# Kernel tuning notes

Measured on AMD Instinct MI355X. Metric: run time of the kernel, lower is better.

## Reference

```python
import jax, jax.numpy as jnp
import numpy as np

N = 10000          # num nodes
E = 640000         # num edges (avg degree 64)
IN_CH = 128
OUT_CH = 128


def setup_inputs() -> dict:
    key = jax.random.key(0)
    k_x, k_ei, k_ea, k_w1, k_b1, k_w2, k_b2 = jax.random.split(key, 7)
    x = jax.random.normal(k_x, (N, IN_CH), dtype=jnp.float32)
    edge_index = jax.random.randint(k_ei, (2, E), 0, N, dtype=jnp.int64)
    edge_attr = jax.random.uniform(k_ea, (E,), dtype=jnp.float32)
    # MLP params: Linear(2*in, out) -> ReLU -> Linear(out, out), stored as [in, out]
    s1 = 1.0 / np.sqrt(2 * IN_CH)
    s2 = 1.0 / np.sqrt(OUT_CH)
    W1 = jax.random.uniform(k_w1, (2 * IN_CH, OUT_CH), jnp.float32, -s1, s1)
    b1 = jax.random.uniform(k_b1, (OUT_CH,), jnp.float32, -s1, s1)
    W2 = jax.random.uniform(k_w2, (OUT_CH, OUT_CH), jnp.float32, -s2, s2)
    b2 = jax.random.uniform(k_b2, (OUT_CH,), jnp.float32, -s2, s2)
    return {"x": x, "edge_index": edge_index, "edge_attr": edge_attr,
            "W1": W1, "b1": b1, "W2": W2, "b2": b2}


def reference(x, edge_index, edge_attr, W1, b1, W2, b2):
    row, col = edge_index[0], edge_index[1]
    # message: scale sender feature by edge_attr, concat with receiver feature, 2-layer MLP
    x_i = x[row] * edge_attr[:, None]          # [E, in]
    x_j = x[col]                               # [E, in]
    combined = jnp.concatenate([x_i, x_j], axis=1)  # [E, 2*in]
    h = jax.nn.relu(combined @ W1 + b1)        # [E, out]
    messages = h @ W2 + b2                     # [E, out]
    # sum aggregation: scatter-add messages into receiving nodes (col)
    out = jnp.zeros((x.shape[0], messages.shape[1]), dtype=messages.dtype)
    out = out.at[col].add(messages)
    return out
```

## Files before the change

### kernel.cpp

```cpp
#include <hip/hip_runtime.h>

#define C 128
#define NPB 16
#define CAP 128
#define OVF_MAX 65536
#define EPT1 16
#define GSH 5
#define G (1 << GSH)
#define CAPB 3072
#define MAXBIN 512

__device__ __forceinline__ unsigned bf16_bits(float x) {
    unsigned u = __float_as_uint(x);
    u += 0x7FFFu + ((u >> 16) & 1u);
    return u >> 16;
}
__device__ __forceinline__ float bf16f(unsigned short b) {
    return __uint_as_float(((unsigned)b) << 16);
}

__global__ void fused_pre_kernel(const float* __restrict__ x, const float* __restrict__ W1,
                                 unsigned short* __restrict__ P16, float* __restrict__ Q,
                                 const int* __restrict__ ei, const float* __restrict__ attr,
                                 uint2* __restrict__ bins, int* __restrict__ bin_cursor,
                                 int* __restrict__ ovf_cnt, int2* __restrict__ ovf,
                                 int N, int E, int PBLK, int NBIN) {
    if ((int)blockIdx.x < PBLK) {
        __shared__ int hist[MAXBIN];
        __shared__ int boff[MAXBIN];
        for (int i = threadIdx.x; i < NBIN; i += 256) { hist[i] = 0; boff[i] = 0; }
        __syncthreads();
        const int base = ((int)blockIdx.x * 256 + (int)threadIdx.x) * EPT1;
        const int rem = (base < E) ? min(EPT1, E - base) : 0;
        const bool vec = (rem == EPT1) && ((E & 3) == 0);
        if (vec) {
#pragma unroll
            for (int j0 = 0; j0 < EPT1; j0 += 4) {
                const int4 c = *(const int4*)(ei + (size_t)E + base + j0);
                atomicAdd(&hist[c.x >> GSH], 1);
                atomicAdd(&hist[c.y >> GSH], 1);
                atomicAdd(&hist[c.z >> GSH], 1);
                atomicAdd(&hist[c.w >> GSH], 1);
            }
        } else {
            for (int j = 0; j < rem; ++j)
                atomicAdd(&hist[ei[(size_t)E + base + j] >> GSH], 1);
        }
        __syncthreads();
        for (int i = threadIdx.x; i < NBIN; i += 256) {
            const int c = hist[i];
            int b = 0;
            if (c) {
                const int cp = (c + 7) & ~7;
                b = atomicAdd(&bin_cursor[i], cp);
                for (int k = c; k < cp; ++k)
                    if (b + k < CAPB)
                        bins[(size_t)i * CAPB + b + k] = make_uint2(0u, 0xFFFFFFFFu);
            }
            hist[i] = b;
        }
        __syncthreads();
        if (vec) {
#pragma unroll
            for (int j0 = 0; j0 < EPT1; j0 += 4) {
                const int4 r = *(const int4*)(ei + base + j0);
                const int4 c = *(const int4*)(ei + (size_t)E + base + j0);
                const float4 a = *(const float4*)(attr + base + j0);
                const int rr[4] = {r.x, r.y, r.z, r.w};
                const int cc[4] = {c.x, c.y, c.z, c.w};
                const float aa[4] = {a.x, a.y, a.z, a.w};
#pragma unroll
                for (int j = 0; j < 4; ++j) {
                    const int bin = cc[j] >> GSH;
                    const int idx = hist[bin] + atomicAdd(&boff[bin], 1);
                    const unsigned pk = (bf16_bits(aa[j]) << 16) | (unsigned)rr[j];
                    if (idx < CAPB) {
                        bins[(size_t)bin * CAPB + idx] = make_uint2(pk, (unsigned)cc[j]);
                    } else {
                        const int o = atomicAdd(ovf_cnt, 1);
                        if (o < OVF_MAX) ovf[o] = make_int2(cc[j], (int)pk);
                    }
                }
            }
        } else {
            for (int j = 0; j < rem; ++j) {
                const int row = ei[base + j], colv = ei[(size_t)E + base + j];
                const int bin = colv >> GSH;
                const int idx = hist[bin] + atomicAdd(&boff[bin], 1);
                const unsigned pk = (bf16_bits(attr[base + j]) << 16) | (unsigned)row;
                if (idx < CAPB) {
                    bins[(size_t)bin * CAPB + idx] = make_uint2(pk, (unsigned)colv);
                } else {
                    const int o = atomicAdd(ovf_cnt, 1);
                    if (o < OVF_MAX) ovf[o] = make_int2(colv, (int)pk);
                }
            }
        }
    } else {
        __shared__ float xs[NPB][C];
        const int pb = (int)blockIdx.x - PBLK;
        const int n0 = pb * NPB;
        const int tt = threadIdx.x & (C - 1);
        const int half = threadIdx.x >> 7;
        for (int i = threadIdx.x; i < NPB * C; i += 256) {
            const int gi = n0 * C + i;
            xs[0][i] = (gi < N * C) ? x[gi] : 0.f;
        }
        __syncthreads();
        const float* __restrict__ Wb = W1 + (half ? (C * C) : 0) + tt;
        float acc[NPB] = {};
        for (int k = 0; k < C; ++k) {
            const float w = Wb[k * C];
#pragma unroll
            for (int j = 0; j < NPB; ++j)
                acc[j] = fmaf(xs[j][k], w, acc[j]);
        }
#pragma unroll
        for (int j = 0; j < NPB; ++j)
            if (n0 + j < N) {
                if (half) Q[(size_t)(n0 + j) * C + tt] = acc[j];
                else      P16[(size_t)(n0 + j) * C + tt] = (unsigned short)bf16_bits(acc[j]);
            }
    }
}

__global__ void bin_scatter_kernel(const uint2* __restrict__ bins, const int* __restrict__ bin_cursor,
                                   unsigned* __restrict__ sorted, int* __restrict__ cursor,
                                   int* __restrict__ ovf_cnt, int2* __restrict__ ovf, int N) {
    __shared__ int off[G];
    const int b = blockIdx.x;
    const int n0 = b << GSH;
    if (threadIdx.x < G) off[threadIdx.x] = 0;
    __syncthreads();
    const int cnt = min(bin_cursor[b], CAPB);
    const uint2* __restrict__ src = bins + (size_t)b * CAPB;
    for (int i = threadIdx.x; i < cnt; i += 256) {
        const uint2 e = src[i];
        const unsigned noff = e.y - (unsigned)n0;
        if (noff < (unsigned)G) {
            const int pos = atomicAdd(&off[noff], 1);
            if (pos < CAP) {
                sorted[(size_t)e.y * CAP + pos] = e.x;
            } else {
                const int o = atomicAdd(ovf_cnt, 1);
                if (o < OVF_MAX) ovf[o] = make_int2((int)e.y, (int)e.x);
            }
        }
    }
    __syncthreads();
    if (threadIdx.x < G && n0 + (int)threadIdx.x < N)
        cursor[n0 + threadIdx.x] = min(off[threadIdx.x], CAP);
}

__global__ void agg_out_kernel(const unsigned* __restrict__ sorted, const int* __restrict__ cursor,
                               const unsigned short* __restrict__ P16, const float* __restrict__ Q,
                               const float* __restrict__ b1, const float* __restrict__ W2,
                               const float* __restrict__ b2,
                               const int* __restrict__ ovf_cnt, const int2* __restrict__ ovf,
                               float* __restrict__ out, int N) {
    __shared__ float4 part[2][4][32];
    __shared__ float hs[2][C];
    const int t = threadIdx.x;
    const int j = t >> 7;
    const int slice = (t >> 5) & 3;
    const int ch4 = t & 31;
    const int n = blockIdx.x * 2 + j;

    float4 acc = make_float4(0.f, 0.f, 0.f, 0.f);
    float4 qb = acc;
    int deg = 0;
    int mcnt = 0;
    if (n < N) {
        deg = cursor[n];
        const float4 q4  = *(const float4*)(Q + (size_t)n * C + (ch4 << 2));
        const float4 b14 = *(const float4*)(b1 + (ch4 << 2));
        qb = make_float4(q4.x + b14.x, q4.y + b14.y, q4.z + b14.z, q4.w + b14.w);
        const int cnt = min(deg, CAP);
        const unsigned* __restrict__ buf = sorted + (size_t)n * CAP;
        const int chunk = (cnt + 3) >> 2;
        const int s0 = min(slice * chunk, cnt);
        const int s1 = min(s0 + chunk, cnt);
        int i = s0;
        for (; i + 4 <= s1; i += 4) {
            const unsigned v0 = buf[i], v1 = buf[i + 1], v2 = buf[i + 2], v3 = buf[i + 3];
            const ushort4 p0 = *(const ushort4*)(P16 + (((size_t)(v0 & 0xFFFFu)) << 7) + (ch4 << 2));
            const ushort4 p1 = *(const ushort4*)(P16 + (((size_t)(v1 & 0xFFFFu)) << 7) + (ch4 << 2));
            const ushort4 p2 = *(const ushort4*)(P16 + (((size_t)(v2 & 0xFFFFu)) << 7) + (ch4 << 2));
            const ushort4 p3 = *(const ushort4*)(P16 + (((size_t)(v3 & 0xFFFFu)) << 7) + (ch4 << 2));
            const float a0 = __uint_as_float(v0 & 0xFFFF0000u);
            const float a1 = __uint_as_float(v1 & 0xFFFF0000u);
            const float a2 = __uint_as_float(v2 & 0xFFFF0000u);
            const float a3 = __uint_as_float(v3 & 0xFFFF0000u);
            acc.x += fmaxf(fmaf(a0, bf16f(p0.x), qb.x), 0.f) + fmaxf(fmaf(a1, bf16f(p1.x), qb.x), 0.f)
                   + fmaxf(fmaf(a2, bf16f(p2.x), qb.x), 0.f) + fmaxf(fmaf(a3, bf16f(p3.x), qb.x), 0.f);
            acc.y += fmaxf(fmaf(a0, bf16f(p0.y), qb.y), 0.f) + fmaxf(fmaf(a1, bf16f(p1.y), qb.y), 0.f)
                   + fmaxf(fmaf(a2, bf16f(p2.y), qb.y), 0.f) + fmaxf(fmaf(a3, bf16f(p3.y), qb.y), 0.f);
            acc.z += fmaxf(fmaf(a0, bf16f(p0.z), qb.z), 0.f) + fmaxf(fmaf(a1, bf16f(p1.z), qb.z), 0.f)
                   + fmaxf(fmaf(a2, bf16f(p2.z), qb.z), 0.f) + fmaxf(fmaf(a3, bf16f(p3.z), qb.z), 0.f);
            acc.w += fmaxf(fmaf(a0, bf16f(p0.w), qb.w), 0.f) + fmaxf(fmaf(a1, bf16f(p1.w), qb.w), 0.f)
                   + fmaxf(fmaf(a2, bf16f(p2.w), qb.w), 0.f) + fmaxf(fmaf(a3, bf16f(p3.w), qb.w), 0.f);
        }
        for (; i < s1; ++i) {
            const unsigned v = buf[i];
            const ushort4 p = *(const ushort4*)(P16 + (((size_t)(v & 0xFFFFu)) << 7) + (ch4 << 2));
            const float a = __uint_as_float(v & 0xFFFF0000u);
            acc.x += fmaxf(fmaf(a, bf16f(p.x), qb.x), 0.f);
            acc.y += fmaxf(fmaf(a, bf16f(p.y), qb.y), 0.f);
            acc.z += fmaxf(fmaf(a, bf16f(p.z), qb.z), 0.f);
            acc.w += fmaxf(fmaf(a, bf16f(p.w), qb.w), 0.f);
        }
        if (slice == 0) {
            const int oc = min(*ovf_cnt, OVF_MAX);
            for (int o = 0; o < oc; ++o) {
                const int2 v = ovf[o];
                if (v.x == n) {
                    ++mcnt;
                    const unsigned u = (unsigned)v.y;
                    const ushort4 p = *(const ushort4*)(P16 + (((size_t)(u & 0xFFFFu)) << 7) + (ch4 << 2));
                    const float a = __uint_as_float(u & 0xFFFF0000u);
                    acc.x += fmaxf(fmaf(a, bf16f(p.x), qb.x), 0.f);
                    acc.y += fmaxf(fmaf(a, bf16f(p.y), qb.y), 0.f);
                    acc.z += fmaxf(fmaf(a, bf16f(p.z), qb.z), 0.f);
                    acc.w += fmaxf(fmaf(a, bf16f(p.w), qb.w), 0.f);
                }
            }
        }
    }
    part[j][slice][ch4] = acc;
    __syncthreads();
    if (slice == 0 && n < N) {
        const float4 r0 = part[j][0][ch4], r1 = part[j][1][ch4];
        const float4 r2 = part[j][2][ch4], r3 = part[j][3][ch4];
        float4 h;
        h.x = r0.x + r1.x + r2.x + r3.x;
        h.y = r0.y + r1.y + r2.y + r3.y;
        h.z = r0.z + r1.z + r2.z + r3.z;
        h.w = r0.w + r1.w + r2.w + r3.w;
        *(float4*)(&hs[j][ch4 << 2]) = h;
    }
    __syncthreads();
    float4 o = make_float4(0.f, 0.f, 0.f, 0.f);
    if (n < N) {
        const int k0 = slice << 5;
#pragma unroll 8
        for (int k = k0; k < k0 + 32; ++k) {
            const float hv = hs[j][k];
            const float4 w = *(const float4*)(W2 + (size_t)k * C + (ch4 << 2));
            o.x = fmaf(hv, w.x, o.x);
            o.y = fmaf(hv, w.y, o.y);
            o.z = fmaf(hv, w.z, o.z);
            o.w = fmaf(hv, w.w, o.w);
        }
    }
    __syncthreads();
    part[j][slice][ch4] = o;
    __syncthreads();
    if (slice == 0 && n < N) {
        const float4 r0 = part[j][0][ch4], r1 = part[j][1][ch4];
        const float4 r2 = part[j][2][ch4], r3 = part[j][3][ch4];
        const float4 b24 = *(const float4*)(b2 + (ch4 << 2));
        const float d = (float)(deg + mcnt);
        float4 res;
        res.x = fmaf(d, b24.x, r0.x + r1.x + r2.x + r3.x);
        res.y = fmaf(d, b24.y, r0.y + r1.y + r2.y + r3.y);
        res.z = fmaf(d, b24.z, r0.z + r1.z + r2.z + r3.z);
        res.w = fmaf(d, b24.w, r0.w + r1.w + r2.w + r3.w);
        *(float4*)(out + (size_t)n * C + (ch4 << 2)) = res;
    }
}

extern "C" void kernel_launch(void* const* d_in, const int* in_sizes, int n_in,
                              void* d_out, int out_size, void* d_ws, size_t ws_size,
                              hipStream_t stream) {
    const float* x    = (const float*)d_in[0];
    const int*   ei   = (const int*)d_in[1];
    const float* attr = (const float*)d_in[2];
    const float* W1   = (const float*)d_in[3];
    const float* b1   = (const float*)d_in[4];
    const float* W2   = (const float*)d_in[5];
    const float* b2   = (const float*)d_in[6];
    float* out = (float*)d_out;

    const int N = in_sizes[0] / C;
    const int E = in_sizes[2];
    const int NBIN = (N + G - 1) >> GSH;

    char* ws = (char*)d_ws;
    unsigned short* P16 = (unsigned short*)ws;  ws += (size_t)N * C * sizeof(unsigned short);
    ws = (char*)(((uintptr_t)ws + 15) & ~(uintptr_t)15);
    float*    Q       = (float*)ws;     ws += (size_t)N * C * sizeof(float);
    unsigned* sorted  = (unsigned*)ws;  ws += (size_t)N * CAP * sizeof(unsigned);
    uint2*    bins    = (uint2*)ws;     ws += (size_t)NBIN * CAPB * sizeof(uint2);
    int2*     ovf     = (int2*)ws;      ws += (size_t)OVF_MAX * sizeof(int2);
    int*      cursor  = (int*)ws;       ws += (size_t)N * sizeof(int);
    int*      bin_cursor = (int*)ws;    ws += (size_t)NBIN * sizeof(int);
    int*      ovf_cnt = (int*)ws;

    hipMemsetAsync(bin_cursor, 0, ((size_t)NBIN + 1) * sizeof(int), stream);

    const int PBLK = (E + 256 * EPT1 - 1) / (256 * EPT1);
    const int PB = (N + NPB - 1) / NPB;
    fused_pre_kernel<<<PBLK + PB, 256, 0, stream>>>(x, W1, P16, Q, ei, attr,
                                                    bins, bin_cursor, ovf_cnt, ovf,
                                                    N, E, PBLK, NBIN);
    bin_scatter_kernel<<<NBIN, 256, 0, stream>>>(bins, bin_cursor, sorted, cursor,
                                                 ovf_cnt, ovf, N);
    agg_out_kernel<<<(N + 1) / 2, 256, 0, stream>>>(sorted, cursor, P16, Q, b1, W2, b2,
                                                    ovf_cnt, ovf, out, N);
}
```

Baseline: 143.0 us.

## Split aggregation and W2 GEMM into separate kernels with wider gathers

Moves the per-node W2 projection out of the aggregation kernel into a separate tiled GEMM kernel that handles 16 nodes per block and reuses each W2 load across 8 rows. The aggregation kernel now stages the node's edge list in shared memory and gathers 8 bf16 channels per thread with 16-byte loads, using 8 edge groups instead of 4. This removes the per-node re-read of all of W2 and the extra barriers in the old fused tail. In exchange it adds an intermediate H buffer round trip through global memory and one more kernel launch.

Measured after the change: 137.3 us. -4.0%, faster.

```diff
diff --git a/kernel.cpp b/kernel.cpp
--- a/kernel.cpp
+++ b/kernel.cpp
@@ -14,9 +14,6 @@
     unsigned u = __float_as_uint(x);
     u += 0x7FFFu + ((u >> 16) & 1u);
     return u >> 16;
-}
-__device__ __forceinline__ float bf16f(unsigned short b) {
-    return __uint_as_float(((unsigned)b) << 16);
 }
 
 __global__ void fused_pre_kernel(const float* __restrict__ x, const float* __restrict__ W1,
@@ -152,120 +149,140 @@
         cursor[n0 + threadIdx.x] = min(off[threadIdx.x], CAP);
 }
 
-__global__ void agg_out_kernel(const unsigned* __restrict__ sorted, const int* __restrict__ cursor,
-                               const unsigned short* __restrict__ P16, const float* __restrict__ Q,
-                               const float* __restrict__ b1, const float* __restrict__ W2,
-                               const float* __restrict__ b2,
-                               const int* __restrict__ ovf_cnt, const int2* __restrict__ ovf,
-                               float* __restrict__ out, int N) {
-    __shared__ float4 part[2][4][32];
-    __shared__ float hs[2][C];
+__global__ void agg_kernel(const unsigned* __restrict__ sorted, const int* __restrict__ cursor,
+                           const unsigned short* __restrict__ P16, const float* __restrict__ Q,
+                           const float* __restrict__ b1,
+                           const int* __restrict__ ovf_cnt, const int2* __restrict__ ovf,
+                           float* __restrict__ H, int* __restrict__ degw, int N) {
+    __shared__ unsigned ebuf[2][CAP];
+    __shared__ float4 red[2][8][32];
     const int t = threadIdx.x;
     const int j = t >> 7;
-    const int slice = (t >> 5) & 3;
-    const int ch4 = t & 31;
+    const int tl = t & 127;
+    const int grp = tl >> 4;
+    const int ch8 = t & 15;
     const int n = blockIdx.x * 2 + j;
 
-    float4 acc = make_float4(0.f, 0.f, 0.f, 0.f);
-    float4 qb = acc;
-    int deg = 0;
-    int mcnt = 0;
+    int deg = 0, cnt = 0, mcnt = 0;
     if (n < N) {
         deg = cursor[n];
-        const float4 q4  = *(const float4*)(Q + (size_t)n * C + (ch4 << 2));
-        const float4 b14 = *(const float4*)(b1 + (ch4 << 2));
-        qb = make_float4(q4.x + b14.x, q4.y + b14.y, q4.z + b14.z, q4.w + b14.w);
-        const int cnt = min(deg, CAP);
-        const unsigned* __restrict__ buf = sorted + (size_t)n * CAP;
-        const int chunk = (cnt + 3) >> 2;
-        const int s0 = min(slice * chunk, cnt);
+        cnt = min(deg, CAP);
+        for (int i = tl; i < cnt; i += 128)
+            ebuf[j][i] = sorted[(size_t)n * CAP + i];
+    }
+    __syncthreads();
+
+    float4 acc0 = make_float4(0.f, 0.f, 0.f, 0.f);
+    float4 acc1 = acc0;
+    if (n < N) {
+        const float4 qlo = *(const float4*)(Q + (size_t)n * C + (ch8 << 3));
+        const float4 qhi = *(const float4*)(Q + (size_t)n * C + (ch8 << 3) + 4);
+        const float4 blo = *(const float4*)(b1 + (ch8 << 3));
+        const float4 bhi = *(const float4*)(b1 + (ch8 << 3) + 4);
+        const float4 qb0 = make_float4(qlo.x + blo.x, qlo.y + blo.y, qlo.z + blo.z, qlo.w + blo.w);
+        const float4 qb1 = make_float4(qhi.x + bhi.x, qhi.y + bhi.y, qhi.z + bhi.z, qhi.w + bhi.w);
+        const int chunk = (cnt + 7) >> 3;
+        const int s0 = min(grp * chunk, cnt);
         const int s1 = min(s0 + chunk, cnt);
         int i = s0;
-        for (; i + 4 <= s1; i += 4) {
-            const unsigned v0 = buf[i], v1 = buf[i + 1], v2 = buf[i + 2], v3 = buf[i + 3];
-            const ushort4 p0 = *(const ushort4*)(P16 + (((size_t)(v0 & 0xFFFFu)) << 7) + (ch4 << 2));
-            const ushort4 p1 = *(const ushort4*)(P16 + (((size_t)(v1 & 0xFFFFu)) << 7) + (ch4 << 2));
-            const ushort4 p2 = *(const ushort4*)(P16 + (((size_t)(v2 & 0xFFFFu)) << 7) + (ch4 << 2));
-            const ushort4 p3 = *(const ushort4*)(P16 + (((size_t)(v3 & 0xFFFFu)) << 7) + (ch4 << 2));
-            const float a0 = __uint_as_float(v0 & 0xFFFF0000u);
-            const float a1 = __uint_as_float(v1 & 0xFFFF0000u);
-            const float a2 = __uint_as_float(v2 & 0xFFFF0000u);
-            const float a3 = __uint_as_float(v3 & 0xFFFF0000u);
-            acc.x += fmaxf(fmaf(a0, bf16f(p0.x), qb.x), 0.f) + fmaxf(fmaf(a1, bf16f(p1.x), qb.x), 0.f)
-                   + fmaxf(fmaf(a2, bf16f(p2.x), qb.x), 0.f) + fmaxf(fmaf(a3, bf16f(p3.x), qb.x), 0.f);
-            acc.y += fmaxf(fmaf(a0, bf16f(p0.y), qb.y), 0.f) + fmaxf(fmaf(a1, bf16f(p1.y), qb.y), 0.f)
-                   + fmaxf(fmaf(a2, bf16f(p2.y), qb.y), 0.f) + fmaxf(fmaf(a3, bf16f(p3.y), qb.y), 0.f);
-            acc.z += fmaxf(fmaf(a0, bf16f(p0.z), qb.z), 0.f) + fmaxf(fmaf(a1, bf16f(p1.z), qb.z), 0.f)
-                   + fmaxf(fmaf(a2, bf16f(p2.z), qb.z), 0.f) + fmaxf(fmaf(a3, bf16f(p3.z), qb.z), 0.f);
-            acc.w += fmaxf(fmaf(a0, bf16f(p0.w), qb.w), 0.f) + fmaxf(fmaf(a1, bf16f(p1.w), qb.w), 0.f)
-                   + fmaxf(fmaf(a2, bf16f(p2.w), qb.w), 0.f) + fmaxf(fmaf(a3, bf16f(p3.w), qb.w), 0.f);
+        for (; i + 2 <= s1; i += 2) {
+            const unsigned e0 = ebuf[j][i], e1 = ebuf[j][i + 1];
+            const uint4 p0 = *(const uint4*)(P16 + (((size_t)(e0 & 0xFFFFu)) << 7) + (ch8 << 3));
+            const uint4 p1 = *(const uint4*)(P16 + (((size_t)(e1 & 0xFFFFu)) << 7) + (ch8 << 3));
+            const float a0 = __uint_as_float(e0 & 0xFFFF0000u);
+            const float a1 = __uint_as_float(e1 & 0xFFFF0000u);
+            acc0.x += fmaxf(fmaf(a0, __uint_as_float(p0.x << 16),         qb0.x), 0.f)
+                    + fmaxf(fmaf(a1, __uint_as_float(p1.x << 16),         qb0.x), 0.f);
+            acc0.y += fmaxf(fmaf(a0, __uint_as_float(p0.x & 0xFFFF0000u), qb0.y), 0.f)
+                    + fmaxf(fmaf(a1, __uint_as_float(p1.x & 0xFFFF0000u), qb0.y), 0.f);
+            acc0.z += fmaxf(fmaf(a0, __uint_as_float(p0.y << 16),         qb0.z), 0.f)
+                    + fmaxf(fmaf(a1, __uint_as_float(p1.y << 16),         qb0.z), 0.f);
+            acc0.w += fmaxf(fmaf(a0, __uint_as_float(p0.y & 0xFFFF0000u), qb0.w), 0.f)
+                    + fmaxf(fmaf(a1, __uint_as_float(p1.y & 0xFFFF0000u), qb0.w), 0.f);
+            acc1.x += fmaxf(fmaf(a0, __uint_as_float(p0.z << 16),         qb1.x), 0.f)
+                    + fmaxf(fmaf(a1, __uint_as_float(p1.z << 16),         qb1.x), 0.f);
+            acc1.y += fmaxf(fmaf(a0, __uint_as_float(p0.z & 0xFFFF0000u), qb1.y), 0.f)
+                    + fmaxf(fmaf(a1, __uint_as_float(p1.z & 0xFFFF0000u), qb1.y), 0.f);
+            acc1.z += fmaxf(fmaf(a0, __uint_as_float(p0.w << 16),         qb1.z), 0.f)
+                    + fmaxf(fmaf(a1, __uint_as_float(p1.w << 16),         qb1.z), 0.f);
+            acc1.w += fmaxf(fmaf(a0, __uint_as_float(p0.w & 0xFFFF0000u), qb1.w), 0.f)
+                    + fmaxf(fmaf(a1, __uint_as_float(p1.w & 0xFFFF0000u), qb1.w), 0.f);
         }
         for (; i < s1; ++i) {
-            const unsigned v = buf[i];
-            const ushort4 p = *(const ushort4*)(P16 + (((size_t)(v & 0xFFFFu)) << 7) + (ch4 << 2));
-            const float a = __uint_as_float(v & 0xFFFF0000u);
-            acc.x += fmaxf(fmaf(a, bf16f(p.x), qb.x), 0.f);
-            acc.y += fmaxf(fmaf(a, bf16f(p.y), qb.y), 0.f);
-            acc.z += fmaxf(fmaf(a, bf16f(p.z), qb.z), 0.f);
-            acc.w += fmaxf(fmaf(a, bf16f(p.w), qb.w), 0.f);
-        }
-        if (slice == 0) {
+            const unsigned e0 = ebuf[j][i];
+            const uint4 p0 = *(const uint4*)(P16 + (((size_t)(e0 & 0xFFFFu)) << 7) + (ch8 << 3));
+            const float a0 = __uint_as_float(e0 & 0xFFFF0000u);
+            acc0.x += fmaxf(fmaf(a0, __uint_as_float(p0.x << 16),         qb0.x), 0.f);
+            acc0.y += fmaxf(fmaf(a0, __uint_as_float(p0.x & 0xFFFF0000u), qb0.y), 0.f);
+            acc0.z += fmaxf(fmaf(a0, __uint_as_float(p0.y << 16),         qb0.z), 0.f);
+            acc0.w += fmaxf(fmaf(a0, __uint_as_float(p0.y & 0xFFFF0000u), qb0.w), 0.f);
+            acc1.x += fmaxf(fmaf(a0, __uint_as_float(p0.z << 16),         qb1.x), 0.f);
+            acc1.y += fmaxf(fmaf(a0, __uint_as_float(p0.z & 0xFFFF0000u), qb1.y), 0.f);
+            acc1.z += fmaxf(fmaf(a0, __uint_as_float(p0.w << 16),         qb1.z), 0.f);
+            acc1.w += fmaxf(fmaf(a0, __uint_as_float(p0.w & 0xFFFF0000u), qb1.w), 0.f);
+        }
+        if (grp == 0) {
             const int oc = min(*ovf_cnt, OVF_MAX);
             for (int o = 0; o < oc; ++o) {
                 const int2 v = ovf[o];
                 if (v.x == n) {
                     ++mcnt;
                     const unsigned u = (unsigned)v.y;
-                    const ushort4 p = *(const ushort4*)(P16 + (((size_t)(u & 0xFFFFu)) << 7) + (ch4 << 2));
-                    const float a = __uint_as_float(u & 0xFFFF0000u);
-                    acc.x += fmaxf(fmaf(a, bf16f(p.x), qb.x), 0.f);
-                    acc.y += fmaxf(fmaf(a, bf16f(p.y), qb.y), 0.f);
-                    acc.z += fmaxf(fmaf(a, bf16f(p.z), qb.z), 0.f);
-                    acc.w += fmaxf(fmaf(a, bf16f(p.w), qb.w), 0.f);
+                    const uint4 p0 = *(const uint4*)(P16 + (((size_t)(u & 0xFFFFu)) << 7) + (ch8 << 3));
+                    const float a0 = __uint_as_float(u & 0xFFFF0000u);
+                    acc0.x += fmaxf(fmaf(a0, __uint_as_float(p0.x << 16),         qb0.x), 0.f);
+                    acc0.y += fmaxf(fmaf(a0, __uint_as_float(p0.x & 0xFFFF0000u), qb0.y), 0.f);
+                    acc0.z += fmaxf(fmaf(a0, __uint_as_float(p0.y << 16),         qb0.z), 0.f);
+                    acc0.w += fmaxf(fmaf(a0, __uint_as_float(p0.y & 0xFFFF0000u), qb0.w), 0.f);
+                    acc1.x += fmaxf(fmaf(a0, __uint_as_float(p0.z << 16),         qb1.x), 0.f);
+                    acc1.y += fmaxf(fmaf(a0, __uint_as_float(p0.z & 0xFFFF0000u), qb1.y), 0.f);
+                    acc1.z += fmaxf(fmaf(a0, __uint_as_float(p0.w << 16),         qb1.z), 0.f);
+                    acc1.w += fmaxf(fmaf(a0, __uint_as_float(p0.w & 0xFFFF0000u), qb1.w), 0.f);
                 }
             }
         }
     }
-    part[j][slice][ch4] = acc;
-    __syncthreads();
-    if (slice == 0 && n < N) {
-        const float4 r0 = part[j][0][ch4], r1 = part[j][1][ch4];
-        const float4 r2 = part[j][2][ch4], r3 = part[j][3][ch4];
-        float4 h;
-        h.x = r0.x + r1.x + r2.x + r3.x;
-        h.y = r0.y + r1.y + r2.y + r3.y;
-        h.z = r0.z + r1.z + r2.z + r3.z;
-        h.w = r0.w + r1.w + r2.w + r3.w;
-        *(float4*)(&hs[j][ch4 << 2]) = h;
-    }
-    __syncthreads();
-    float4 o = make_float4(0.f, 0.f, 0.f, 0.f);
+    red[j][grp][(ch8 << 1)]     = acc0;
+    red[j][grp][(ch8 << 1) | 1] = acc1;
+    __syncthreads();
     if (n < N) {
-        const int k0 = slice << 5;
-#pragma unroll 8
-        for (int k = k0; k < k0 + 32; ++k) {
-            const float hv = hs[j][k];
-            const float4 w = *(const float4*)(W2 + (size_t)k * C + (ch4 << 2));
-            o.x = fmaf(hv, w.x, o.x);
-            o.y = fmaf(hv, w.y, o.y);
-            o.z = fmaf(hv, w.z, o.z);
-            o.w = fmaf(hv, w.w, o.w);
-        }
-    }
-    __syncthreads();
-    part[j][slice][ch4] = o;
-    __syncthreads();
-    if (slice == 0 && n < N) {
-        const float4 r0 = part[j][0][ch4], r1 = part[j][1][ch4];
-        const float4 r2 = part[j][2][ch4], r3 = part[j][3][ch4];
-        const float4 b24 = *(const float4*)(b2 + (ch4 << 2));
-        const float d = (float)(deg + mcnt);
-        float4 res;
-        res.x = fmaf(d, b24.x, r0.x + r1.x + r2.x + r3.x);
-        res.y = fmaf(d, b24.y, r0.y + r1.y + r2.y + r3.y);
-        res.z = fmaf(d, b24.z, r0.z + r1.z + r2.z + r3.z);
-        res.w = fmaf(d, b24.w, r0.w + r1.w + r2.w + r3.w);
-        *(float4*)(out + (size_t)n * C + (ch4 << 2)) = res;
+        if (tl == 0) degw[n] = deg + mcnt;
+        if (tl < 32) {
+            float4 s = red[j][0][tl];
+#pragma unroll
+            for (int g = 1; g < 8; ++g) {
+                const float4 r = red[j][g][tl];
+                s.x += r.x; s.y += r.y; s.z += r.z; s.w += r.w;
+            }
+            *(float4*)(H + (size_t)n * C + (tl << 2)) = s;
+        }
+    }
+}
+
+__global__ void out_gemm_kernel(const float* __restrict__ H, const float* __restrict__ W2,
+                                const float* __restrict__ b2, const int* __restrict__ degw,
+                                float* __restrict__ out, int N) {
+    __shared__ float hsm[NPB][C];
+    const int n0 = (int)blockIdx.x * NPB;
+    const int col = threadIdx.x & (C - 1);
+    const int half = threadIdx.x >> 7;
+    for (int i = threadIdx.x; i < NPB * C; i += 256) {
+        const int gi = n0 * C + i;
+        hsm[0][i] = (gi < N * C) ? H[gi] : 0.f;
+    }
+    __syncthreads();
+    float acc[8] = {};
+    for (int k = 0; k < C; ++k) {
+        const float w = W2[k * C + col];
+#pragma unroll
+        for (int j = 0; j < 8; ++j)
+            acc[j] = fmaf(hsm[half * 8 + j][k], w, acc[j]);
+    }
+    const float bv = b2[col];
+#pragma unroll
+    for (int j = 0; j < 8; ++j) {
+        const int n = n0 + half * 8 + j;
+        if (n < N) out[(size_t)n * C + col] = fmaf((float)degw[n], bv, acc[j]);
     }
 }
 
@@ -289,10 +306,12 @@
     unsigned short* P16 = (unsigned short*)ws;  ws += (size_t)N * C * sizeof(unsigned short);
     ws = (char*)(((uintptr_t)ws + 15) & ~(uintptr_t)15);
     float*    Q       = (float*)ws;     ws += (size_t)N * C * sizeof(float);
+    float*    H       = (float*)ws;     ws += (size_t)N * C * sizeof(float);
     unsigned* sorted  = (unsigned*)ws;  ws += (size_t)N * CAP * sizeof(unsigned);
     uint2*    bins    = (uint2*)ws;     ws += (size_t)NBIN * CAPB * sizeof(uint2);
     int2*     ovf     = (int2*)ws;      ws += (size_t)OVF_MAX * sizeof(int2);
     int*      cursor  = (int*)ws;       ws += (size_t)N * sizeof(int);
+    int*      degw    = (int*)ws;       ws += (size_t)N * sizeof(int);
     int*      bin_cursor = (int*)ws;    ws += (size_t)NBIN * sizeof(int);
     int*      ovf_cnt = (int*)ws;
 
@@ -305,6 +324,7 @@
                                                     N, E, PBLK, NBIN);
     bin_scatter_kernel<<<NBIN, 256, 0, stream>>>(bins, bin_cursor, sorted, cursor,
                                                  ovf_cnt, ovf, N);
-    agg_out_kernel<<<(N + 1) / 2, 256, 0, stream>>>(sorted, cursor, P16, Q, b1, W2, b2,
-                                                    ovf_cnt, ovf, out, N);
-}
+    agg_kernel<<<(N + 1) / 2, 256, 0, stream>>>(sorted, cursor, P16, Q, b1,
+                                                ovf_cnt, ovf, H, degw, N);
+    out_gemm_kernel<<<(N + NPB - 1) / NPB, 256, 0, stream>>>(H, W2, b2, degw, out, N);
+}
```
